# Optimization experiments

Measured on AMD Instinct MI355X. Metric: run time of the kernel, lower is better.

The kernel has to match this reference:

```python
import jax, jax.numpy as jnp
import numpy as np

NUM_LEVELS = 8
NODES_PER_LEVEL = 16384
CHILDREN_PER_NODE = 8
DIM = 64


def _build_layered_dag():
    rng = np.random.default_rng(0)
    srcs, dsts = [], []
    for lvl in range(NUM_LEVELS - 1):
        child_base = lvl * NODES_PER_LEVEL
        parent_base = (lvl + 1) * NODES_PER_LEVEL
        children = rng.integers(0, NODES_PER_LEVEL, size=(NODES_PER_LEVEL, CHILDREN_PER_NODE)) + child_base
        parents = np.repeat(np.arange(NODES_PER_LEVEL) + parent_base, CHILDREN_PER_NODE)
        srcs.append(children.ravel())
        dsts.append(parents)
    ei = np.stack([np.concatenate(srcs), np.concatenate(dsts)]).astype(np.int32)
    return jnp.asarray(ei)


def setup_inputs() -> dict:
    key = jax.random.key(0)
    k1, k2, k3, k4 = jax.random.split(key, 4)
    N = NUM_LEVELS * NODES_PER_LEVEL
    x = jax.random.normal(k1, (N, DIM), dtype=jnp.float32)
    edge_index = _build_layered_dag()
    s = 1.0 / np.sqrt(DIM)
    W_l = jax.random.uniform(k2, (DIM, DIM), jnp.float32, -s, s)
    b_l = jax.random.uniform(k3, (DIM,), jnp.float32, -s, s)
    W_r = jax.random.uniform(k4, (DIM, DIM), jnp.float32, -s, s)
    return {"x": x, "edge_index": edge_index, "W_l": W_l, "b_l": b_l,
            "W_r": W_r, "num_levels": NUM_LEVELS}


def reference(x, edge_index, W_l, b_l, W_r, num_levels):
    N, d = x.shape
    src, dst = edge_index[0], edge_index[1]
    E = src.shape[0]

    # in-degree; leaves have no incoming edges
    indeg = jax.ops.segment_sum(jnp.ones((E,), jnp.int32), dst, num_segments=N)
    leaves = indeg == 0                                   # [N] bool

    out = jnp.where(leaves[:, None], jnp.tanh(x), 0.0)    # out[leaves] = tanh(x[leaves])
    visited = leaves

    # root_weight path: overwrite rows of out where x row is nonzero
    row_nonzero = jnp.any(x != 0, axis=1)
    out = jnp.where(row_nonzero[:, None], x @ W_r.T, out)

    prev = leaves  # previous_visits as boolean node mask
    for _ in range(num_levels - 1):
        mask_e = prev[src]                                # edges from previous front
        acv = jax.ops.segment_sum((visited[src] & mask_e).astype(jnp.int32), dst, num_segments=N)
        tc = jax.ops.segment_sum(mask_e.astype(jnp.int32), dst, num_segments=N)
        fathers = tc > 0
        ref_next = fathers & (acv == tc)                  # parents with all children visited

        m2 = ref_next[dst]
        agg = jax.ops.segment_sum(jnp.where(m2[:, None], out[src], 0.0), dst, num_segments=N)
        upd = agg @ W_l.T + b_l
        out = jnp.where(ref_next[:, None], jnp.tanh(out + upd), out)
        visited = visited | ref_next
        prev = ref_next
    return out
```

## Files before the change

### kernel.cpp

```cpp
#include <hip/hip_runtime.h>

#define NPL   16384
#define DIM   64
#define CPN   8
#define EPL   (NPL * CPN)
#define NLEV  8

#define TPB     512
#define WPB     (TPB / 64)
#define CBLOCKS 256
#define NPB     (NPL / CBLOCKS)
#define NPW     (NPB / WPB)

__device__ __forceinline__ void co_st(float* p, float v) {
    __hip_atomic_store(p, v, __ATOMIC_RELAXED, __HIP_MEMORY_SCOPE_AGENT);
}

__device__ __forceinline__ void load_wrow(float* dst, const float* W, int row) {
    const float4* p = (const float4*)(W + row * DIM);
    #pragma unroll
    for (int q = 0; q < DIM / 4; ++q) {
        float4 v = p[q];
        dst[4*q+0] = v.x; dst[4*q+1] = v.y;
        dst[4*q+2] = v.z; dst[4*q+3] = v.w;
    }
}

__device__ __forceinline__ float fast_tanh(float z) {
    z = fminf(15.f, fmaxf(-15.f, z));
    float e = __expf(-2.f * z);
    return (1.f - e) * __builtin_amdgcn_rcpf(1.f + e);
}

__device__ __forceinline__ void gridbar(int* cnt, int target) {
    __syncthreads();
    if (threadIdx.x == 0) {
        __hip_atomic_fetch_add(cnt, 1, __ATOMIC_RELAXED,
                               __HIP_MEMORY_SCOPE_AGENT);
        while (__hip_atomic_load(cnt, __ATOMIC_RELAXED,
                                 __HIP_MEMORY_SCOPE_AGENT) < target)
            __builtin_amdgcn_s_sleep(2);
    }
    asm volatile("" ::: "memory");
    __syncthreads();
}

template<bool COH>
__device__ __forceinline__ void phaseA(
    const float* __restrict__ x, const float* __restrict__ Wr,
    float* __restrict__ out, float* __restrict__ XR,
    int lane, int w, int blk, float* sX4)
{
    constexpr int GPL = NPW / 4;
    constexpr int NG  = NLEV * GPL;

    float wr[DIM];
    load_wrow(wr, Wr, lane);

    const int base = blk * NPB + w * NPW;
    const int sub  = lane >> 4;
    const int col4 = (lane & 15) * 4;

    float4 q0, q1, q2;
    #define ROWB(g) ((long)((g) / GPL) * NPL + base + ((g) % GPL) * 4)
    q0 = *(const float4*)&x[(ROWB(0) + sub) * DIM + col4];
    q1 = *(const float4*)&x[(ROWB(1) + sub) * DIM + col4];

    #pragma unroll
    for (int g = 0; g < NG; ++g) {
        if (g + 2 < NG)
            q2 = *(const float4*)&x[(ROWB(g + 2) + sub) * DIM + col4];

        *(float4*)&sX4[sub * DIM + col4] = q0;

        const long rb = ROWB(g);
        const int  L  = g / GPL;
        #pragma unroll
        for (int rr = 0; rr < 4; ++rr) {
            float a0 = 0.f, a1 = 0.f, a2 = 0.f, a3 = 0.f;
            const float4* A = (const float4*)&sX4[rr * DIM];
            #pragma unroll
            for (int k = 0; k < DIM / 4; ++k) {
                float4 av = A[k];
                a0 += av.x * wr[4*k+0];
                a1 += av.y * wr[4*k+1];
                a2 += av.z * wr[4*k+2];
                a3 += av.w * wr[4*k+3];
            }
            float r = (a0 + a1) + (a2 + a3);
            const long gg = rb + rr;
            if (L == 0) {
                float* d = &out[gg * DIM + lane];
                if (COH) co_st(d, r); else *d = r;
            } else {
                XR[gg * DIM + lane] = r;
            }
        }
        q0 = q1; q1 = q2;
    }
    #undef ROWB
}

template<bool COH>
__device__ __forceinline__ void phaseB(
    int vidx, const float* __restrict__ XR, float* __restrict__ out,
    const float* wl, float bias, int L, int lane, int w, int blk, float* sA)
{
    const int  pbase = blk * NPB + w * NPW;
    const long gbase = (long)L * NPL;

    float g[4][CPN];
    float xr[4];

    #define ISSUE(c, s)                                                       \
        {                                                                     \
            _Pragma("unroll")                                                 \
            for (int j = 0; j < CPN; ++j) {                                   \
                int si = __builtin_amdgcn_readlane(vidx, (c) * CPN + j);      \
                g[s][j] = out[(long)si * DIM + lane];      \
            }                                                                 \
            xr[s] = XR[(gbase + pbase + (c)) * DIM + lane];                   \
        }

    ISSUE(0, 0);
    ISSUE(1, 1);
    ISSUE(2, 2);

    #pragma unroll
    for (int c = 0; c < NPW; ++c) {
        const int slot = c & 3;
        if (c + 3 < NPW) ISSUE(c + 3, (c + 3) & 3);

        float s0 = g[slot][0] + g[slot][1];
        float s1 = g[slot][2] + g[slot][3];
        float s2 = g[slot][4] + g[slot][5];
        float s3 = g[slot][6] + g[slot][7];
        float agg = (s0 + s1) + (s2 + s3);
        sA[lane] = agg;

        float a0 = 0.f, a1 = 0.f, a2 = 0.f, a3 = bias + xr[slot];
        const float4* B = (const float4*)sA;
        #pragma unroll
        for (int k = 0; k < DIM / 4; ++k) {
            float4 bv = B[k];
            a0 += bv.x * wl[4*k+0];
            a1 += bv.y * wl[4*k+1];
            a2 += bv.z * wl[4*k+2];
            a3 += bv.w * wl[4*k+3];
        }
        float r = fast_tanh((a0 + a1) + (a2 + a3));
        float* d = &out[(gbase + pbase + c) * DIM + lane];
        if (COH) co_st(d, r); else *d = r;
    }
    #undef ISSUE
}

__global__ __launch_bounds__(TPB, 2) void dag_fused(
    const float* __restrict__ x, const int* __restrict__ src,
    const float* __restrict__ Wl, const float* __restrict__ bl,
    const float* __restrict__ Wr, float* __restrict__ out,
    float* __restrict__ ws)
{
    __shared__ __align__(16) float sbuf[WPB][256];

    const int lane = threadIdx.x & 63;
    const int w    = threadIdx.x >> 6;

    int*   barcnt = (int*)ws;
    float* XR     = ws + 64;

    const int pbase = blockIdx.x * NPB + w * NPW;
    int vidx[NLEV - 1];
    #pragma unroll
    for (int L = 1; L < NLEV; ++L)
        vidx[L - 1] = src[(long)(L - 1) * EPL + pbase * CPN + lane];

    phaseA<true>(x, Wr, out, XR, lane, w, blockIdx.x, sbuf[w]);
    gridbar(barcnt, CBLOCKS);

    float wl[DIM];
    load_wrow(wl, Wl, lane);
    const float bias = bl[lane];

    #pragma unroll
    for (int L = 1; L < NLEV; ++L) {
        phaseB<true>(vidx[L - 1], XR, out, wl, bias, L, lane, w,
                     blockIdx.x, sbuf[w]);
        if (L + 1 < NLEV)
            gridbar(barcnt, (L + 1) * CBLOCKS);
    }
}

__global__ __launch_bounds__(TPB) void dag_phaseA_k(
    const float* __restrict__ x, const float* __restrict__ Wr,
    float* __restrict__ out, float* __restrict__ ws)
{
    __shared__ __align__(16) float sbuf[WPB][256];
    const int lane = threadIdx.x & 63;
    const int w    = threadIdx.x >> 6;
    phaseA<false>(x, Wr, out, ws + 64, lane, w, blockIdx.x, sbuf[w]);
}

__global__ __launch_bounds__(TPB) void dag_phaseB_k(
    const int* __restrict__ src, const float* __restrict__ Wl,
    const float* __restrict__ bl, float* __restrict__ out,
    float* __restrict__ ws, int L)
{
    __shared__ __align__(16) float sbuf[WPB][256];
    const int lane = threadIdx.x & 63;
    const int w    = threadIdx.x >> 6;
    const int pbase = blockIdx.x * NPB + w * NPW;
    int vidx = src[(long)(L - 1) * EPL + pbase * CPN + lane];
    float wl[DIM];
    load_wrow(wl, Wl, lane);
    phaseB<false>(vidx, ws + 64, out, wl, bl[lane], L, lane, w,
                  blockIdx.x, sbuf[w]);
}

extern "C" void kernel_launch(void* const* d_in, const int* in_sizes, int n_in,
                              void* d_out, int out_size, void* d_ws, size_t ws_size,
                              hipStream_t stream) {
    const float* x  = (const float*)d_in[0];
    const int*   ei = (const int*)d_in[1];
    const float* Wl = (const float*)d_in[2];
    const float* bl = (const float*)d_in[3];
    const float* Wr = (const float*)d_in[4];
    float* out = (float*)d_out;
    float* ws  = (float*)d_ws;

    const int* src = ei;

    hipMemsetAsync(ws, 0, 256, stream);

    void* args[] = {(void*)&x, (void*)&src, (void*)&Wl, (void*)&bl,
                    (void*)&Wr, (void*)&out, (void*)&ws};
    hipError_t e = hipLaunchCooperativeKernel((const void*)dag_fused,
                                              dim3(CBLOCKS), dim3(TPB),
                                              args, 0, stream);
    if (e != hipSuccess) {
        (void)hipGetLastError();
        hipLaunchKernelGGL(dag_phaseA_k, dim3(CBLOCKS), dim3(TPB), 0, stream,
                           x, Wr, out, ws);
        for (int L = 1; L < NLEV; ++L) {
            hipLaunchKernelGGL(dag_phaseB_k, dim3(CBLOCKS), dim3(TPB), 0, stream,
                               src, Wl, bl, out, ws, L);
        }
    }
}
```

Before: 223.7 us.

## Replace contended grid barrier with per-block flags and early arrival

Replaces the single-counter grid barrier with per-block arrival counters padded to separate cache lines. One wavefront of block 0 polls all 256 counters and then publishes a release flag, which the other blocks spin on in groups of 32. In phase A each block signals arrival as soon as its level-0 rows are written, before it computes the XR projections for the other levels. This lets the first barrier overlap that remaining work and cuts atomic contention on a single address. The cost is an extra hop through block 0 and larger workspace initialisation, and the spin loops now give up after a fixed cap.

```diff
diff --git a/kernel.cpp b/kernel.cpp
--- a/kernel.cpp
+++ b/kernel.cpp
@@ -12,6 +12,9 @@
 #define NPB     (NPL / CBLOCKS)
 #define NPW     (NPB / WPB)
 
+#define SPIN_CAP (1 << 24)
+
+
 __device__ __forceinline__ void co_st(float* p, float v) {
     __hip_atomic_store(p, v, __ATOMIC_RELAXED, __HIP_MEMORY_SCOPE_AGENT);
 }
@@ -32,24 +35,56 @@
     return (1.f - e) * __builtin_amdgcn_rcpf(1.f + e);
 }
 
-__device__ __forceinline__ void gridbar(int* cnt, int target) {
+__device__ __forceinline__ void bar_arrive(int* wsI) {
     __syncthreads();
-    if (threadIdx.x == 0) {
-        __hip_atomic_fetch_add(cnt, 1, __ATOMIC_RELAXED,
+    if (threadIdx.x == 0)
+        __hip_atomic_fetch_add(wsI + blockIdx.x * 16, 1, __ATOMIC_RELAXED,
                                __HIP_MEMORY_SCOPE_AGENT);
-        while (__hip_atomic_load(cnt, __ATOMIC_RELAXED,
-                                 __HIP_MEMORY_SCOPE_AGENT) < target)
-            __builtin_amdgcn_s_sleep(2);
+}
+
+__device__ __forceinline__ void bar_wait(int* wsI, int round) {
+    const int tgt = round + 1;
+    if (blockIdx.x == 0) {
+        if (threadIdx.x < 64) {
+            const int l = threadIdx.x;
+            int* a0 = wsI + l * 16;
+            int* a1 = wsI + (l + 64) * 16;
+            int* a2 = wsI + (l + 128) * 16;
+            int* a3 = wsI + (l + 192) * 16;
+            for (int it = 0; it < SPIN_CAP; ++it) {
+                int m0 = __hip_atomic_load(a0, __ATOMIC_RELAXED,
+                                           __HIP_MEMORY_SCOPE_AGENT);
+                int m1 = __hip_atomic_load(a1, __ATOMIC_RELAXED,
+                                           __HIP_MEMORY_SCOPE_AGENT);
+                int m2 = __hip_atomic_load(a2, __ATOMIC_RELAXED,
+                                           __HIP_MEMORY_SCOPE_AGENT);
+                int m3 = __hip_atomic_load(a3, __ATOMIC_RELAXED,
+                                           __HIP_MEMORY_SCOPE_AGENT);
+                bool ok = (m0 >= tgt) & (m1 >= tgt) & (m2 >= tgt) & (m3 >= tgt);
+                if (__ballot(ok) == ~0ull) break;
+                __builtin_amdgcn_s_sleep(1);
+            }
+            if (l < 8)
+                __hip_atomic_store(wsI + 4096 + l * 64, tgt, __ATOMIC_RELAXED,
+                                   __HIP_MEMORY_SCOPE_AGENT);
+        }
+    } else if (threadIdx.x == 0) {
+        int* rel = wsI + 4096 + (blockIdx.x >> 5) * 64;
+        for (int it = 0; it < SPIN_CAP; ++it) {
+            if (__hip_atomic_load(rel, __ATOMIC_RELAXED,
+                                  __HIP_MEMORY_SCOPE_AGENT) >= tgt) break;
+            __builtin_amdgcn_s_sleep(1);
+        }
     }
     asm volatile("" ::: "memory");
     __syncthreads();
 }
 
-template<bool COH>
+template<bool COH, bool SB>
 __device__ __forceinline__ void phaseA(
     const float* __restrict__ x, const float* __restrict__ Wr,
     float* __restrict__ out, float* __restrict__ XR,
-    int lane, int w, int blk, float* sX4)
+    int lane, int w, int blk, float* sX4, int* wsI)
 {
     constexpr int GPL = NPW / 4;
     constexpr int NG  = NLEV * GPL;
@@ -97,6 +132,9 @@
             }
         }
         q0 = q1; q1 = q2;
+
+        if (SB && g == GPL - 1)
+            bar_arrive(wsI);
     }
     #undef ROWB
 }
@@ -166,8 +204,8 @@
     const int lane = threadIdx.x & 63;
     const int w    = threadIdx.x >> 6;
 
-    int*   barcnt = (int*)ws;
-    float* XR     = ws + 64;
+    int*   wsI = (int*)ws;
+    float* XR  = ws + 8192;
 
     const int pbase = blockIdx.x * NPB + w * NPW;
     int vidx[NLEV - 1];
@@ -175,8 +213,8 @@
     for (int L = 1; L < NLEV; ++L)
         vidx[L - 1] = src[(long)(L - 1) * EPL + pbase * CPN + lane];
 
-    phaseA<true>(x, Wr, out, XR, lane, w, blockIdx.x, sbuf[w]);
-    gridbar(barcnt, CBLOCKS);
+    phaseA<true, true>(x, Wr, out, XR, lane, w, blockIdx.x, sbuf[w], wsI);
+    bar_wait(wsI, 0);
 
     float wl[DIM];
     load_wrow(wl, Wl, lane);
@@ -186,8 +224,10 @@
     for (int L = 1; L < NLEV; ++L) {
         phaseB<true>(vidx[L - 1], XR, out, wl, bias, L, lane, w,
                      blockIdx.x, sbuf[w]);
-        if (L + 1 < NLEV)
-            gridbar(barcnt, (L + 1) * CBLOCKS);
+        if (L + 1 < NLEV) {
+            bar_arrive(wsI);
+            bar_wait(wsI, L);
+        }
     }
 }
 
@@ -198,7 +238,8 @@
     __shared__ __align__(16) float sbuf[WPB][256];
     const int lane = threadIdx.x & 63;
     const int w    = threadIdx.x >> 6;
-    phaseA<false>(x, Wr, out, ws + 64, lane, w, blockIdx.x, sbuf[w]);
+    phaseA<false, false>(x, Wr, out, ws + 8192, lane, w, blockIdx.x,
+                         sbuf[w], nullptr);
 }
 
 __global__ __launch_bounds__(TPB) void dag_phaseB_k(
@@ -213,7 +254,7 @@
     int vidx = src[(long)(L - 1) * EPL + pbase * CPN + lane];
     float wl[DIM];
     load_wrow(wl, Wl, lane);
-    phaseB<false>(vidx, ws + 64, out, wl, bl[lane], L, lane, w,
+    phaseB<false>(vidx, ws + 8192, out, wl, bl[lane], L, lane, w,
                   blockIdx.x, sbuf[w]);
 }
 
@@ -230,7 +271,7 @@
 
     const int* src = ei;
 
-    hipMemsetAsync(ws, 0, 256, stream);
+    hipMemsetAsync(ws, 0, 32768, stream);
 
     void* args[] = {(void*)&x, (void*)&src, (void*)&Wl, (void*)&bl,
                     (void*)&Wr, (void*)&out, (void*)&ws};
```

Result: faster. 196.0 us (-12.4%).
